# Performance work log

Measured on AMD Instinct MI355X. Metric: run time of the kernel, lower is better.

Reference implementation:

```python
import jax, jax.numpy as jnp
import numpy as np
import math

ALPHA_MIN = math.exp(-1.0 / 5.0)   # ~0.8187
ALPHA_MAX = math.exp(-1.0 / 25.0)  # ~0.9608
THRESHOLD = 1.0


def setup_inputs() -> dict:
    key = jax.random.key(0)
    k1, k2, k3, k4, k5 = jax.random.split(key, 5)
    B, T, I, H = 32, 2048, 256, 512
    x = jax.random.normal(k1, (B, T, I), dtype=jnp.float32)
    # Linear weight, kaiming-ish scale
    W = jax.random.normal(k2, (H, I), dtype=jnp.float32) * (1.0 / np.sqrt(I))
    # alpha ~ U[exp(-1/5), exp(-1/25)] as in nn.init.uniform_
    alpha = ALPHA_MIN + jax.random.uniform(k3, (H,), dtype=jnp.float32) * (ALPHA_MAX - ALPHA_MIN)
    # initial membrane potential / spike state (torch.rand in _lif_cell)
    u0 = jax.random.uniform(k4, (B, H), dtype=jnp.float32)
    s0 = jax.random.uniform(k5, (B, H), dtype=jnp.float32)
    return {"x": x, "W": W, "alpha": alpha, "u0": u0, "s0": s0}


def reference(x, W, alpha, u0, s0):
    # clamp alpha to its admissible range (lif_feature has no 'NoClamp')
    alpha = jnp.clip(alpha, ALPHA_MIN, ALPHA_MAX)
    b = 1.0 - alpha  # lif_feature has no 'B'

    # feedforward projection: [B, T, H]
    Wx = jnp.einsum('bti,hi->bth', x, W)

    def step(carry, wx_t):
        ut, st = carry
        ut = alpha * (ut - st) + b * wx_t          # leaky integrate + soft reset
        st = (ut - THRESHOLD > 0).astype(ut.dtype)  # heaviside spike
        return (ut, st), st

    # scan over time: Wx -> [T, B, H]
    _, s = jax.lax.scan(step, (u0, s0), jnp.swapaxes(Wx, 0, 1))
    return jnp.swapaxes(s, 0, 1)  # [B, T, H]
```

## Files before the change

### kernel.cpp

```cpp
#include <hip/hip_runtime.h>

#define ALPHA_MIN 0.8187307530779818f
#define ALPHA_MAX 0.9607894391523232f

typedef _Float16 f16;
typedef _Float16 f16x4 __attribute__((ext_vector_type(4)));
typedef _Float16 f16x8 __attribute__((ext_vector_type(8)));
typedef float f32x16 __attribute__((ext_vector_type(16)));

#define BB_ 32
#define TT_ 2048
#define KK_ 256
#define HH_ 512
#define TC_ 64
#define NC_ 32
#define KH_ 128

__device__ __forceinline__ void barrier_lds() {
    __builtin_amdgcn_s_waitcnt(0xC07F);
    __builtin_amdgcn_s_barrier();
}

__global__ __launch_bounds__(448, 1) void lif_fused5(
    const float* __restrict__ X,
    const float* __restrict__ W,
    const float* __restrict__ alpha,
    const float* __restrict__ u0,
    const float* __restrict__ s0,
    float* __restrict__ out)
{
    __shared__ f16 Ah[2][TC_ * KH_];
    __shared__ f16 Al[2][TC_ * KH_];
    __shared__ float wxbuf[2][TC_ * 64];

    const int b  = blockIdx.x & 31;
    const int nt = blockIdx.x >> 5;
    const int n0 = nt * 64;

    const int tid  = threadIdx.x;
    const int wv   = tid >> 6;
    const int lane = tid & 63;
    const int fm   = lane & 31;
    const int fq   = lane >> 5;

    if (wv < 4) {
        const int mh = wv >> 1;
        const int nh = wv & 1;

        f16x8 bh[16], bl[16];
        {
            const float* wp = W + (size_t)(n0 + nh * 32 + fm) * KK_ + fq * 8;
#pragma unroll
            for (int ks = 0; ks < 16; ++ks) {
                float4 v0 = *(const float4*)(wp + ks * 16);
                float4 v1 = *(const float4*)(wp + ks * 16 + 4);
                float v[8] = {v0.x, v0.y, v0.z, v0.w, v1.x, v1.y, v1.z, v1.w};
                f16x8 h, l;
#pragma unroll
                for (int j = 0; j < 8; ++j) {
                    const f16 hj = (f16)v[j];
                    h[j] = hj;
                    l[j] = (f16)((v[j] - (float)hj) * 2048.0f);
                }
                bh[ks] = h; bl[ks] = l;
            }
        }

        f32x16 accH, accLa, accLb;
#pragma unroll
        for (int e = 0; e < 16; ++e) { accH[e] = 0.0f; accLa[e] = 0.0f; accLb[e] = 0.0f; }

        const int row = mh * 32 + fm;
        const int r15 = row & 15;

        auto compute_half = [&](int hf) {
            __builtin_amdgcn_s_setprio(1);
#pragma unroll
            for (int ks = 0; ks < 8; ++ks) {
                const int addr = row * KH_ + (((ks * 2 + fq) ^ r15) * 8);
                const f16x8 ah = *(const f16x8*)&Ah[hf][addr];
                const f16x8 al = *(const f16x8*)&Al[hf][addr];
                const int ksg = hf * 8 + ks;
                accH  = __builtin_amdgcn_mfma_f32_32x32x16_f16(ah, bh[ksg], accH,  0, 0, 0);
                accLa = __builtin_amdgcn_mfma_f32_32x32x16_f16(ah, bl[ksg], accLa, 0, 0, 0);
                accLb = __builtin_amdgcn_mfma_f32_32x32x16_f16(al, bh[ksg], accLb, 0, 0, 0);
            }
            __builtin_amdgcn_s_setprio(0);
        };

        barrier_lds();
        for (int c = 0; c < NC_; ++c) {
            compute_half(0);
            barrier_lds();
            compute_half(1);
            {
                float* wb = &wxbuf[c & 1][0];
                const int colw = nh * 32 + fm;
#pragma unroll
                for (int r = 0; r < 16; ++r) {
                    const int roww = mh * 32 + (r & 3) + 8 * (r >> 2) + 4 * fq;
                    wb[roww * 64 + colw] = accH[r] + (accLa[r] + accLb[r]) * (1.0f / 2048.0f);
                    accH[r] = 0.0f; accLa[r] = 0.0f; accLb[r] = 0.0f;
                }
            }
            barrier_lds();
        }
    } else if (wv < 6) {
        const int u      = wv - 4;
        const int srow_j = u * 32 + (lane >> 5);
        const int f4i    = lane & 31;
        const int g      = f4i >> 1;
        const int sub    = f4i & 1;

        float4 pend[16];
        auto issue_loads = [&](int c, int kh) {
            const float* base = X + ((size_t)b * TT_ + c * TC_) * KK_ + kh * KH_ + f4i * 4;
#pragma unroll
            for (int j = 0; j < 16; ++j)
                pend[j] = *(const float4*)(base + (size_t)(srow_j + j * 2) * KK_);
        };
        auto cvt_write = [&](int bufi) {
#pragma unroll
            for (int j = 0; j < 16; ++j) {
                const int rowa = srow_j + j * 2;
                const float v[4] = {pend[j].x, pend[j].y, pend[j].z, pend[j].w};
                f16x4 h, l;
#pragma unroll
                for (int e = 0; e < 4; ++e) {
                    const f16 he = (f16)v[e];
                    h[e] = he;
                    l[e] = (f16)((v[e] - (float)he) * 2048.0f);
                }
                const int addr = rowa * KH_ + ((g ^ (rowa & 15)) * 8) + sub * 4;
                *(f16x4*)&Ah[bufi][addr] = h;
                *(f16x4*)&Al[bufi][addr] = l;
            }
        };

        issue_loads(0, 0);
        cvt_write(0);
        issue_loads(0, 1);
        barrier_lds();

        for (int c = 0; c < NC_; ++c) {
            cvt_write(1);
            if (c + 1 < NC_) issue_loads(c + 1, 0);
            barrier_lds();
            if (c + 1 < NC_) { cvt_write(0); issue_loads(c + 1, 1); }
            barrier_lds();
        }
    } else {
        const int h = n0 + lane;
        const int chain = b * HH_ + h;
        float a = alpha[h];
        a = fminf(fmaxf(a, ALPHA_MIN), ALPHA_MAX);
        const float bbv = 1.0f - a;
        float u = u0[chain];
        float s = s0[chain];
        float* op = out + (size_t)b * TT_ * HH_ + h;

        auto consume = [&](int c, int hf) {
            const float* wb = &wxbuf[c & 1][0];
            const int tb = c * TC_ + hf * 32;
#pragma unroll
            for (int t0 = 0; t0 < 32; t0 += 8) {
                float w[8];
#pragma unroll
                for (int j = 0; j < 8; ++j) w[j] = wb[(hf * 32 + t0 + j) * 64 + lane];
#pragma unroll
                for (int j = 0; j < 8; ++j) {
                    u = fmaf(a, u - s, bbv * w[j]);
                    s = (u > 1.0f) ? 1.0f : 0.0f;
                    __builtin_nontemporal_store(s, &op[(size_t)(tb + t0 + j) * HH_]);
                }
            }
        };

        barrier_lds();
        for (int c = 0; c < NC_; ++c) {
            if (c) consume(c - 1, 0);
            barrier_lds();
            if (c) consume(c - 1, 1);
            barrier_lds();
        }
        consume(NC_ - 1, 0);
        consume(NC_ - 1, 1);
    }
}

__global__ void gemm_naive(const float* __restrict__ X, const float* __restrict__ W,
                           float* __restrict__ C, int M, int N, int K)
{
    const int idx = blockIdx.x * 256 + threadIdx.x;
    if (idx >= M * N) return;
    const int m = idx / N, n = idx % N;
    float acc = 0.0f;
    for (int k = 0; k < K; ++k) acc = fmaf(X[(size_t)m * K + k], W[(size_t)n * K + k], acc);
    C[idx] = acc;
}

__global__ __launch_bounds__(64) void lif_scan_inplace(
    float* __restrict__ buf, const float* __restrict__ alpha,
    const float* __restrict__ u0, const float* __restrict__ s0, int T, int H)
{
    const int chain = blockIdx.x * 64 + threadIdx.x;
    const int h = chain % H;
    const int b = chain / H;
    float a = alpha[h];
    a = fminf(fmaxf(a, ALPHA_MIN), ALPHA_MAX);
    const float bb = 1.0f - a;
    float u = u0[chain], s = s0[chain];
    float* base = buf + (size_t)b * T * H + h;
    for (int t = 0; t < T; ++t) {
        u = fmaf(a, u - s, bb * base[(size_t)t * H]);
        s = (u > 1.0f) ? 1.0f : 0.0f;
        base[(size_t)t * H] = s;
    }
}

extern "C" void kernel_launch(void* const* d_in, const int* in_sizes, int n_in,
                              void* d_out, int out_size, void* d_ws, size_t ws_size,
                              hipStream_t stream) {
    const float* x     = (const float*)d_in[0];
    const float* W     = (const float*)d_in[1];
    const float* alpha = (const float*)d_in[2];
    const float* u0    = (const float*)d_in[3];
    const float* s0    = (const float*)d_in[4];
    float* out = (float*)d_out;

    const int H = in_sizes[2];
    const int I = in_sizes[1] / H;
    const int B = in_sizes[3] / H;
    const int T = in_sizes[0] / (B * I);

    if (B == BB_ && T == TT_ && I == KK_ && H == HH_) {
        lif_fused5<<<256, 448, 0, stream>>>(x, W, alpha, u0, s0, out);
    } else {
        const int M = B * T;
        gemm_naive<<<(M * H + 255) / 256, 256, 0, stream>>>(x, W, out, M, H, I);
        lif_scan_inplace<<<(B * H + 63) / 64, 64, 0, stream>>>(out, alpha, u0, s0, T, H);
    }
}
```

Before: 279.9 us.

## Double producer waves and prefetch two half-chunks ahead of X conversion

The X-loading producer role grows from two waves to four, so each wave handles 16 rows per half-chunk instead of 32. Loads are split into two register sets (pA, pB) so the global reads for a half-chunk are issued two steps before they are converted into LDS, deepening the prefetch pipeline. The block grows from 448 to 576 threads, which adds register and scheduling pressure on the CU and leaves the MFMA and scan waves with a smaller share of issue slots.

After: 276.0 us. About the same (-1.4%).

```diff
diff --git a/kernel.cpp b/kernel.cpp
--- a/kernel.cpp
+++ b/kernel.cpp
@@ -21,7 +21,7 @@
     __builtin_amdgcn_s_barrier();
 }
 
-__global__ __launch_bounds__(448, 1) void lif_fused5(
+__global__ __launch_bounds__(576, 1) void lif_fused6(
     const float* __restrict__ X,
     const float* __restrict__ W,
     const float* __restrict__ alpha,
@@ -105,25 +105,34 @@
             }
             barrier_lds();
         }
-    } else if (wv < 6) {
+    } else if (wv < 8) {
         const int u      = wv - 4;
-        const int srow_j = u * 32 + (lane >> 5);
+        const int srow_j = u * 16 + (lane >> 5);
         const int f4i    = lane & 31;
         const int g      = f4i >> 1;
         const int sub    = f4i & 1;
 
-        float4 pend[16];
-        auto issue_loads = [&](int c, int kh) {
+        float4 pA[8], pB[8];
+
+        auto issueA = [&](int hs) {
+            const int c = hs >> 1, kh = hs & 1;
             const float* base = X + ((size_t)b * TT_ + c * TC_) * KK_ + kh * KH_ + f4i * 4;
 #pragma unroll
-            for (int j = 0; j < 16; ++j)
-                pend[j] = *(const float4*)(base + (size_t)(srow_j + j * 2) * KK_);
-        };
-        auto cvt_write = [&](int bufi) {
-#pragma unroll
-            for (int j = 0; j < 16; ++j) {
+            for (int j = 0; j < 8; ++j)
+                pA[j] = *(const float4*)(base + (size_t)(srow_j + j * 2) * KK_);
+        };
+        auto issueB = [&](int hs) {
+            const int c = hs >> 1, kh = hs & 1;
+            const float* base = X + ((size_t)b * TT_ + c * TC_) * KK_ + kh * KH_ + f4i * 4;
+#pragma unroll
+            for (int j = 0; j < 8; ++j)
+                pB[j] = *(const float4*)(base + (size_t)(srow_j + j * 2) * KK_);
+        };
+        auto cvtA = [&](int bufi) {
+#pragma unroll
+            for (int j = 0; j < 8; ++j) {
                 const int rowa = srow_j + j * 2;
-                const float v[4] = {pend[j].x, pend[j].y, pend[j].z, pend[j].w};
+                const float v[4] = {pA[j].x, pA[j].y, pA[j].z, pA[j].w};
                 f16x4 h, l;
 #pragma unroll
                 for (int e = 0; e < 4; ++e) {
@@ -136,17 +145,36 @@
                 *(f16x4*)&Al[bufi][addr] = l;
             }
         };
-
-        issue_loads(0, 0);
-        cvt_write(0);
-        issue_loads(0, 1);
+        auto cvtB = [&](int bufi) {
+#pragma unroll
+            for (int j = 0; j < 8; ++j) {
+                const int rowa = srow_j + j * 2;
+                const float v[4] = {pB[j].x, pB[j].y, pB[j].z, pB[j].w};
+                f16x4 h, l;
+#pragma unroll
+                for (int e = 0; e < 4; ++e) {
+                    const f16 he = (f16)v[e];
+                    h[e] = he;
+                    l[e] = (f16)((v[e] - (float)he) * 2048.0f);
+                }
+                const int addr = rowa * KH_ + ((g ^ (rowa & 15)) * 8) + sub * 4;
+                *(f16x4*)&Ah[bufi][addr] = h;
+                *(f16x4*)&Al[bufi][addr] = l;
+            }
+        };
+
+        issueA(0);
+        issueB(1);
+        cvtA(0);
+        issueA(2);
         barrier_lds();
 
         for (int c = 0; c < NC_; ++c) {
-            cvt_write(1);
-            if (c + 1 < NC_) issue_loads(c + 1, 0);
-            barrier_lds();
-            if (c + 1 < NC_) { cvt_write(0); issue_loads(c + 1, 1); }
+            cvtB(1);
+            if (c < NC_ - 1) issueB(2 * c + 3);
+            barrier_lds();
+            if (c < NC_ - 1) cvtA(0);
+            if (c < NC_ - 2) issueA(2 * c + 4);
             barrier_lds();
         }
     } else {
@@ -234,7 +262,7 @@
     const int T = in_sizes[0] / (B * I);
 
     if (B == BB_ && T == TT_ && I == KK_ && H == HH_) {
-        lif_fused5<<<256, 448, 0, stream>>>(x, W, alpha, u0, s0, out);
+        lif_fused6<<<256, 576, 0, stream>>>(x, W, alpha, u0, s0, out);
     } else {
         const int M = B * T;
         gemm_naive<<<(M * H + 255) / 256, 256, 0, stream>>>(x, W, out, M, H, I);
```
